# Optimization experiments

Measured on AMD Instinct MI355X. Metric: run time of the kernel, lower is better.

Reference implementation:

```python
import jax, jax.numpy as jnp
import numpy as np

B, S, D = 8, 2048, 1024      # batch, seq (tokens), in/out token dim
E = 2 * D                    # expansion dim (expansion_factor=2)
SDIM = 128                   # attention feature dim s
SQRT_S = float(np.sqrt(SDIM))
EPS_LN = 1e-5                # ScaleNorm eps


def setup_inputs() -> dict:
    key = jax.random.key(0)
    ks = jax.random.split(key, 8)
    return {
        "x": jax.random.normal(ks[0], (B, S, D), jnp.float32),
        "pos_enc": jax.random.normal(ks[1], (S, SDIM), jnp.float32),
        "ln_g": jnp.ones((1,), jnp.float32),                                   # ScaleNorm scalar gain
        "uv_w": jax.random.normal(ks[2], (2 * E + SDIM, D), jnp.float32) / np.sqrt(D),  # fused uv proj (xavier-ish)
        "gamma": jax.random.uniform(ks[3], (2, SDIM), jnp.float32),            # q/k affine scale
        "beta": jax.random.uniform(ks[4], (2, SDIM), jnp.float32),             # q/k affine shift
        "o_w": jax.random.normal(ks[5], (D, E), jnp.float32) / np.sqrt(E),     # output proj
        "res_scale": jnp.ones((D,), jnp.float32),                              # ChannelWiseScale
    }


def reference(x, pos_enc, ln_g, uv_w, gamma, beta, o_w, res_scale):
    # ScaleNorm: x / clamp(||x|| * d^-0.5, eps) * g
    norm = jnp.linalg.norm(x, axis=-1, keepdims=True) * (D ** -0.5)
    xn = x / jnp.maximum(norm, EPS_LN) * ln_g
    # fused uv projection + SiLU
    uv = jax.nn.silu(xn @ uv_w.T)                      # [B,S,2E+s]
    u = uv[..., :E]                                    # gate
    v = uv[..., E:2 * E]                               # values
    base = uv[..., 2 * E:]                             # shared q/k base [B,S,s]
    qk_base = base[..., None, :] * gamma + beta        # [B,S,2,s]
    q = qk_base[..., 0, :] + pos_enc                   # add positional enc [B,S,s]
    k = qk_base[..., 1, :] + pos_enc
    # squared-ReLU attention kernel
    kernel = jnp.square(jax.nn.relu(jnp.einsum('bqs,bks->bqk', q, k) / SQRT_S))
    out = (u * jnp.einsum('bqk,bke->bqe', kernel, v)) @ o_w.T  # [B,S,D]
    # channel-wise scaled residual (in_dims == out_dims -> shortcut)
    return x * res_scale + out
```

## Files before the change

### kernel.cpp

```cpp
#include <hip/hip_runtime.h>
#include <stdint.h>

#define B_   8
#define S_   2048
#define D_   1024
#define E_   2048
#define SD_  128
#define M_   (B_ * S_)
#define NUV  (2 * E_ + SD_)

typedef __attribute__((ext_vector_type(8))) short short8;
typedef __attribute__((ext_vector_type(4))) float floatx4;

typedef __attribute__((address_space(1))) void as1_void;
typedef __attribute__((address_space(3))) void as3_void;

__device__ __forceinline__ ushort f2bf(float f) {
    uint32_t u = __float_as_uint(f);
    uint32_t r = (u + 0x7fffu + ((u >> 16) & 1u)) >> 16;
    return (ushort)r;
}
__device__ __forceinline__ float bf2f(ushort h) {
    return __uint_as_float(((uint32_t)h) << 16);
}
__device__ __forceinline__ float silu(float z) {
    return z * __builtin_amdgcn_rcpf(1.0f + __expf(-z));
}

__device__ __forceinline__ void gld_lds16(const ushort* g, ushort* l) {
    __builtin_amdgcn_global_load_lds((const as1_void*)g, (as3_void*)l, 16, 0, 0);
}

__device__ __forceinline__ void tile_swizzle(int& mt, int& nt) {
    const int gx  = gridDim.x;
    const int lin = blockIdx.y * gx + blockIdx.x;
    const int bandSz = gx * 8;
    const int band = lin / bandSz;
    const int rem  = lin - band * bandSz;
    const int full = gx >> 2;
    const int sc   = rem >> 5;
    if (sc < full) {
        const int r2 = rem & 31;
        mt = band * 8 + (r2 & 7);
        nt = sc * 4 + (r2 >> 3);
    } else {
        const int r3 = rem - full * 32;
        mt = band * 8 + (r3 & 7);
        nt = full * 4 + (r3 >> 3);
    }
}

__device__ __forceinline__ void gemm_core(
    const ushort* __restrict__ A, const ushort* __restrict__ B,
    int lda, int ldb, int K, int m0, int n0,
    ushort* ldsA, ushort* ldsB, floatx4 acc[4][4])
{
    const int t    = threadIdx.x;
    const int lane = t & 63;
    const int l15  = lane & 15;
    const int quad = lane >> 4;
    const int wave = t >> 6;
    const int wm   = (wave >> 1) * 64;
    const int wn   = (wave & 1) * 64;
    const int key  = l15 & 7;

    const ushort* gA[4]; const ushort* gB[4];
    ushort* lA[4]; ushort* lB[4];
    #pragma unroll
    for (int i = 0; i < 4; ++i) {
        const int c   = t + i * 256;
        const int row = c >> 3;
        const int gkc = ((c & 7) ^ (row & 7)) * 8;
        gA[i] = A + (size_t)(m0 + row) * lda + gkc;
        gB[i] = B + (size_t)(n0 + row) * ldb + gkc;
        lA[i] = ldsA + c * 8;
        lB[i] = ldsB + c * 8;
    }

    for (int kk = 0; kk < K; kk += 64) {
        __syncthreads();
        #pragma unroll
        for (int i = 0; i < 4; ++i) gld_lds16(gA[i] + kk, lA[i]);
        #pragma unroll
        for (int i = 0; i < 4; ++i) gld_lds16(gB[i] + kk, lB[i]);
        __syncthreads();

        #pragma unroll
        for (int s = 0; s < 2; ++s) {
            const int koff = ((s * 4 + quad) ^ key) * 8;
            short8 af[4], bfr[4];
            #pragma unroll
            for (int mi = 0; mi < 4; ++mi)
                af[mi] = *(const short8*)(ldsA + (wm + mi * 16 + l15) * 64 + koff);
            #pragma unroll
            for (int ni = 0; ni < 4; ++ni)
                bfr[ni] = *(const short8*)(ldsB + (wn + ni * 16 + l15) * 64 + koff);
            #pragma unroll
            for (int mi = 0; mi < 4; ++mi)
                #pragma unroll
                for (int ni = 0; ni < 4; ++ni)
                    acc[mi][ni] = __builtin_amdgcn_mfma_f32_16x16x32_bf16(
                        af[mi], bfr[ni], acc[mi][ni], 0, 0, 0);
        }
    }
}

#define EPI_INDICES \
    const int t = threadIdx.x; \
    const int lane = t & 63, l15 = lane & 15, quad = lane >> 4; \
    const int wave = t >> 6, wm = (wave >> 1) * 64, wn = (wave & 1) * 64; \
    (void)t;

#define ZERO_ACC \
    floatx4 acc[4][4]; \
    _Pragma("unroll") \
    for (int i = 0; i < 4; ++i) \
        _Pragma("unroll") \
        for (int j = 0; j < 4; ++j) \
            _Pragma("unroll") \
            for (int r = 0; r < 4; ++r) acc[i][j][r] = 0.0f;

__global__ __launch_bounds__(256) void k_cvt(const float* __restrict__ src,
                                             ushort* __restrict__ dst, int n4) {
    int i = blockIdx.x * 256 + threadIdx.x;
    if (i < n4) {
        float4 v = ((const float4*)src)[i];
        ushort4 o;
        o.x = f2bf(v.x); o.y = f2bf(v.y); o.z = f2bf(v.z); o.w = f2bf(v.w);
        ((ushort4*)dst)[i] = o;
    }
}

__global__ __launch_bounds__(256) void k_rmsnorm(const float* __restrict__ x,
                                                 const float* __restrict__ ln_g,
                                                 ushort* __restrict__ xnb) {
    const int m = blockIdx.x;
    const int t = threadIdx.x;
    float4 v = ((const float4*)(x + (size_t)m * D_))[t];
    float ss = v.x * v.x + v.y * v.y + v.z * v.z + v.w * v.w;
    #pragma unroll
    for (int off = 32; off > 0; off >>= 1) ss += __shfl_down(ss, off, 64);
    __shared__ float red[4];
    if ((t & 63) == 0) red[t >> 6] = ss;
    __syncthreads();
    float tot = red[0] + red[1] + red[2] + red[3];
    float rms = sqrtf(tot * (1.0f / (float)D_));
    float scale = ln_g[0] / fmaxf(rms, 1e-5f);
    ushort4 o;
    o.x = f2bf(v.x * scale); o.y = f2bf(v.y * scale);
    o.z = f2bf(v.z * scale); o.w = f2bf(v.w * scale);
    ((ushort4*)(xnb + (size_t)m * D_))[t] = o;
}

__global__ __launch_bounds__(256, 3) void k_gemm1(
    const ushort* __restrict__ xnb, const ushort* __restrict__ uvwb,
    const float* __restrict__ gamma, const float* __restrict__ beta,
    const float* __restrict__ pos,
    ushort* __restrict__ u, ushort* __restrict__ vT,
    ushort* __restrict__ qb, ushort* __restrict__ kb)
{
    __shared__ __align__(16) ushort lds[17408];
    ushort* ldsA = lds;
    ushort* ldsB = lds + 8192;
    ZERO_ACC
    int mt, nt;
    tile_swizzle(mt, nt);
    const int m0 = mt * 128;
    const int n0 = nt * 128;
    gemm_core(xnb, uvwb, D_, D_, D_, m0, n0, ldsA, ldsB, acc);
    EPI_INDICES

    if (nt < 16) {
        #pragma unroll
        for (int mi = 0; mi < 4; ++mi)
            #pragma unroll
            for (int ni = 0; ni < 4; ++ni) {
                const int col = n0 + wn + ni * 16 + l15;
                #pragma unroll
                for (int r = 0; r < 4; ++r) {
                    const int row = m0 + wm + mi * 16 + quad * 4 + r;
                    u[(size_t)row * E_ + col] = f2bf(silu(acc[mi][ni][r]));
                }
            }
    } else if (nt < 32) {
        const int b   = m0 >> 11;
        const int s0  = m0 & (S_ - 1);
        const int ec0 = n0 - E_;
        __syncthreads();
        #pragma unroll
        for (int mi = 0; mi < 4; ++mi)
            #pragma unroll
            for (int ni = 0; ni < 4; ++ni) {
                const int col = wn + ni * 16 + l15;
                const int row = wm + mi * 16 + quad * 4;
                #pragma unroll
                for (int r = 0; r < 4; r += 2) {
                    ushort2 pr;
                    pr.x = f2bf(silu(acc[mi][ni][r]));
                    pr.y = f2bf(silu(acc[mi][ni][r + 1]));
                    *(ushort2*)&lds[col * 136 + row + r] = pr;
                }
            }
        __syncthreads();
        ushort* vTb = vT + ((size_t)b * E_ + ec0) * S_ + s0;
        #pragma unroll
        for (int i = 0; i < 8; ++i) {
            const int lin = i * 256 + t;
            const int e  = lin >> 4;
            const int sb = (lin & 15) * 8;
            *(short8*)(vTb + (size_t)e * S_ + sb) = *(const short8*)&lds[e * 136 + sb];
        }
    } else {
        #pragma unroll
        for (int mi = 0; mi < 4; ++mi)
            #pragma unroll
            for (int ni = 0; ni < 4; ++ni) {
                const int sd = wn + ni * 16 + l15;
                const float g0 = gamma[sd], g1 = gamma[SD_ + sd];
                const float be0 = beta[sd], be1 = beta[SD_ + sd];
                #pragma unroll
                for (int r = 0; r < 4; ++r) {
                    const int row = m0 + wm + mi * 16 + quad * 4 + r;
                    const int srow = row & (S_ - 1);
                    float s = silu(acc[mi][ni][r]);
                    const float p = pos[(size_t)srow * SD_ + sd];
                    qb[(size_t)row * SD_ + sd] = f2bf(s * g0 + be0 + p);
                    kb[(size_t)row * SD_ + sd] = f2bf(s * g1 + be1 + p);
                }
            }
    }
}

__global__ __launch_bounds__(256, 3) void k_scores(
    const ushort* __restrict__ qb, const ushort* __restrict__ kb,
    ushort* __restrict__ kern, int b_off)
{
    __shared__ __align__(16) ushort ldsA[128 * 64];
    __shared__ __align__(16) ushort ldsB[128 * 64];
    ZERO_ACC
    const int bz = blockIdx.z;
    const int b  = b_off + bz;
    int mt, nt;
    tile_swizzle(mt, nt);
    const int m0 = mt * 128;
    const int n0 = nt * 128;
    gemm_core(qb + (size_t)b * S_ * SD_, kb + (size_t)b * S_ * SD_,
              SD_, SD_, SD_, m0, n0, ldsA, ldsB, acc);
    EPI_INDICES
    ushort* ko = kern + (size_t)bz * S_ * S_;
    const float inv = 0.08838834764831845f;
    #pragma unroll
    for (int mi = 0; mi < 4; ++mi)
        #pragma unroll
        for (int ni = 0; ni < 4; ++ni) {
            const int col = n0 + wn + ni * 16 + l15;
            #pragma unroll
            for (int r = 0; r < 4; ++r) {
                const int row = m0 + wm + mi * 16 + quad * 4 + r;
                float s = fmaxf(acc[mi][ni][r] * inv, 0.0f);
                ko[(size_t)row * S_ + col] = f2bf(s * s);
            }
        }
}

__global__ __launch_bounds__(256, 3) void k_kv(
    const ushort* __restrict__ kern, const ushort* __restrict__ vT,
    const ushort* __restrict__ u, ushort* __restrict__ kvu, int b_off)
{
    __shared__ __align__(16) ushort ldsA[128 * 64];
    __shared__ __align__(16) ushort ldsB[128 * 64];
    ZERO_ACC
    const int bz = blockIdx.z;
    const int b  = b_off + bz;
    int mt, nt;
    tile_swizzle(mt, nt);
    const int m0 = mt * 128;
    const int n0 = nt * 128;
    gemm_core(kern + (size_t)bz * S_ * S_, vT + (size_t)b * E_ * S_,
              S_, S_, S_, m0, n0, ldsA, ldsB, acc);
    EPI_INDICES
    #pragma unroll
    for (int mi = 0; mi < 4; ++mi)
        #pragma unroll
        for (int ni = 0; ni < 4; ++ni) {
            const int col = n0 + wn + ni * 16 + l15;
            #pragma unroll
            for (int r = 0; r < 4; ++r) {
                const int row = m0 + wm + mi * 16 + quad * 4 + r;
                const size_t gi = (size_t)(b * S_ + row) * E_ + col;
                float uval = bf2f(u[gi]);
                kvu[gi] = f2bf(uval * acc[mi][ni][r]);
            }
        }
}

__global__ __launch_bounds__(256, 3) void k_out(
    const ushort* __restrict__ kvu, const ushort* __restrict__ owb,
    const float* __restrict__ x, const float* __restrict__ res_scale,
    float* __restrict__ out)
{
    __shared__ __align__(16) ushort ldsA[128 * 64];
    __shared__ __align__(16) ushort ldsB[128 * 64];
    ZERO_ACC
    int mt, nt;
    tile_swizzle(mt, nt);
    const int m0 = mt * 128;
    const int n0 = nt * 128;
    gemm_core(kvu, owb, E_, E_, E_, m0, n0, ldsA, ldsB, acc);
    EPI_INDICES
    #pragma unroll
    for (int mi = 0; mi < 4; ++mi)
        #pragma unroll
        for (int ni = 0; ni < 4; ++ni) {
            const int col = n0 + wn + ni * 16 + l15;
            const float rs = res_scale[col];
            #pragma unroll
            for (int r = 0; r < 4; ++r) {
                const int row = m0 + wm + mi * 16 + quad * 4 + r;
                const size_t gi = (size_t)row * D_ + col;
                out[gi] = x[gi] * rs + acc[mi][ni][r];
            }
        }
}

extern "C" void kernel_launch(void* const* d_in, const int* in_sizes, int n_in,
                              void* d_out, int out_size, void* d_ws, size_t ws_size,
                              hipStream_t stream)
{
    const float* x         = (const float*)d_in[0];
    const float* pos       = (const float*)d_in[1];
    const float* ln_g      = (const float*)d_in[2];
    const float* uv_w      = (const float*)d_in[3];
    const float* gamma     = (const float*)d_in[4];
    const float* beta      = (const float*)d_in[5];
    const float* o_w       = (const float*)d_in[6];
    const float* res_scale = (const float*)d_in[7];
    float* out = (float*)d_out;

    char* p = (char*)d_ws;
    ushort* region0 = (ushort*)p; p += (size_t)M_ * D_ * 2;
    ushort* uvwb    = (ushort*)p; p += (size_t)NUV * D_ * 2;
    ushort* owb     = (ushort*)p; p += (size_t)D_ * E_ * 2;
    ushort* u       = (ushort*)p; p += (size_t)M_ * E_ * 2;
    ushort* kvu     = (ushort*)p; p += (size_t)M_ * E_ * 2;
    ushort* vT      = (ushort*)p; p += (size_t)M_ * E_ * 2;
    ushort* qb      = (ushort*)p; p += (size_t)M_ * SD_ * 2;
    ushort* kb      = (ushort*)p; p += (size_t)M_ * SD_ * 2;

    ushort* xnb  = region0;
    ushort* kern = region0;

    k_cvt<<<(NUV * D_ / 4 + 255) / 256, 256, 0, stream>>>(uv_w, uvwb, NUV * D_ / 4);
    k_cvt<<<(D_ * E_ / 4 + 255) / 256, 256, 0, stream>>>(o_w, owb, D_ * E_ / 4);
    k_rmsnorm<<<M_, 256, 0, stream>>>(x, ln_g, xnb);
    k_gemm1<<<dim3(NUV / 128, M_ / 128), 256, 0, stream>>>(xnb, uvwb, gamma, beta, pos, u, vT, qb, kb);
    for (int g = 0; g < 2; ++g) {
        k_scores<<<dim3(S_ / 128, S_ / 128, 4), 256, 0, stream>>>(qb, kb, kern, g * 4);
        k_kv<<<dim3(E_ / 128, S_ / 128, 4), 256, 0, stream>>>(kern, vT, u, kvu, g * 4);
    }
    k_out<<<dim3(D_ / 128, M_ / 128), 256, 0, stream>>>(kvu, owb, x, res_scale, out);
}
```

Baseline: 576.8 us.

## Switch all GEMMs to 256x256 tiles with double-buffered 8-wave ping-pong pipeline

Replaces the 128x128 single-buffered GEMM core with a 256x256 tile, 512-thread (8-wave) kernel. It double-buffers LDS (128 KB) and interleaves async global-to-LDS loads with MFMA phases, using explicit waitcnt, barriers and setprio. The uv weight is zero-padded to a multiple of 256 rows so the first GEMM tiles evenly, and the epilogues are reworked for the new accumulator layout. The aim is higher arithmetic intensity and hiding load latency behind compute. In exchange, occupancy drops and the grid gets coarser, so tail effects grow, and the hand-tuned waitcnt scheme is fragile.

```diff
diff --git a/kernel.cpp b/kernel.cpp
--- a/kernel.cpp
+++ b/kernel.cpp
@@ -8,6 +8,7 @@
 #define SD_  128
 #define M_   (B_ * S_)
 #define NUV  (2 * E_ + SD_)
+#define NUV2 4352
 
 typedef __attribute__((ext_vector_type(8))) short short8;
 typedef __attribute__((ext_vector_type(4))) float floatx4;
@@ -26,99 +27,136 @@
 __device__ __forceinline__ float silu(float z) {
     return z * __builtin_amdgcn_rcpf(1.0f + __expf(-z));
 }
-
 __device__ __forceinline__ void gld_lds16(const ushort* g, ushort* l) {
     __builtin_amdgcn_global_load_lds((const as1_void*)g, (as3_void*)l, 16, 0, 0);
 }
 
-__device__ __forceinline__ void tile_swizzle(int& mt, int& nt) {
+__device__ __forceinline__ void tile_swizzle4(int& mt, int& nt) {
     const int gx  = gridDim.x;
     const int lin = blockIdx.y * gx + blockIdx.x;
-    const int bandSz = gx * 8;
+    const int bandSz = gx * 4;
     const int band = lin / bandSz;
     const int rem  = lin - band * bandSz;
     const int full = gx >> 2;
-    const int sc   = rem >> 5;
+    const int sc   = rem >> 4;
     if (sc < full) {
-        const int r2 = rem & 31;
-        mt = band * 8 + (r2 & 7);
-        nt = sc * 4 + (r2 >> 3);
+        const int r2 = rem & 15;
+        mt = band * 4 + (r2 & 3);
+        nt = sc * 4 + (r2 >> 2);
     } else {
-        const int r3 = rem - full * 32;
-        mt = band * 8 + (r3 & 7);
-        nt = full * 4 + (r3 >> 3);
-    }
-}
-
-__device__ __forceinline__ void gemm_core(
+        const int r3 = rem - full * 16;
+        mt = band * 4 + (r3 & 3);
+        nt = full * 4 + (r3 >> 2);
+    }
+}
+
+#define STAGE_A(bufn, h, kk) { \
+    gld_lds16(gA0 + (size_t)(h) * a128 + (kk), LA##bufn + (h) * 8192 + t * 8); \
+    gld_lds16(gA1 + (size_t)(h) * a128 + (kk), LA##bufn + (h) * 8192 + t * 8 + 4096); }
+#define STAGE_B(bufn, h, kk) { \
+    gld_lds16(gB0 + (size_t)(h) * b128 + (kk), LB##bufn + (h) * 8192 + t * 8); \
+    gld_lds16(gB1 + (size_t)(h) * b128 + (kk), LB##bufn + (h) * 8192 + t * 8 + 4096); }
+
+#define PHASE(bufn, mq, nq, STAGES, WAITC) { \
+    short8 af_[4][2], bf_[2][2]; \
+    { const ushort* pa_ = LA##bufn + (mq) * 8192 + aoff; \
+      const ushort* pb_ = LB##bufn + (nq) * 8192 + boff; \
+      _Pragma("unroll") \
+      for (int mi_ = 0; mi_ < 4; ++mi_) { \
+          af_[mi_][0] = *(const short8*)(pa_ + mi_ * 1024 + koff0); \
+          af_[mi_][1] = *(const short8*)(pa_ + mi_ * 1024 + koff1); } \
+      _Pragma("unroll") \
+      for (int ni_ = 0; ni_ < 2; ++ni_) { \
+          bf_[ni_][0] = *(const short8*)(pb_ + ni_ * 1024 + koff0); \
+          bf_[ni_][1] = *(const short8*)(pb_ + ni_ * 1024 + koff1); } } \
+    STAGES \
+    __builtin_amdgcn_s_barrier(); \
+    asm volatile("s_waitcnt lgkmcnt(0)" ::: "memory"); \
+    __builtin_amdgcn_sched_barrier(0); \
+    __builtin_amdgcn_s_setprio(1); \
+    _Pragma("unroll") \
+    for (int mi_ = 0; mi_ < 4; ++mi_) \
+        _Pragma("unroll") \
+        for (int ni_ = 0; ni_ < 2; ++ni_) { \
+            acc[mq][nq][mi_][ni_] = __builtin_amdgcn_mfma_f32_16x16x32_bf16( \
+                af_[mi_][0], bf_[ni_][0], acc[mq][nq][mi_][ni_], 0, 0, 0); \
+            acc[mq][nq][mi_][ni_] = __builtin_amdgcn_mfma_f32_16x16x32_bf16( \
+                af_[mi_][1], bf_[ni_][1], acc[mq][nq][mi_][ni_], 0, 0, 0); } \
+    __builtin_amdgcn_s_setprio(0); \
+    WAITC \
+    __builtin_amdgcn_s_barrier(); }
+
+__device__ __forceinline__ void gemm256(
     const ushort* __restrict__ A, const ushort* __restrict__ B,
     int lda, int ldb, int K, int m0, int n0,
-    ushort* ldsA, ushort* ldsB, floatx4 acc[4][4])
+    ushort* lds, floatx4 (&acc)[2][2][4][2])
 {
     const int t    = threadIdx.x;
     const int lane = t & 63;
     const int l15  = lane & 15;
     const int quad = lane >> 4;
-    const int wave = t >> 6;
-    const int wm   = (wave >> 1) * 64;
-    const int wn   = (wave & 1) * 64;
+    const int w    = t >> 6;
+    const int wr   = w >> 2;
+    const int wc   = w & 3;
     const int key  = l15 & 7;
-
-    const ushort* gA[4]; const ushort* gB[4];
-    ushort* lA[4]; ushort* lB[4];
-    #pragma unroll
-    for (int i = 0; i < 4; ++i) {
-        const int c   = t + i * 256;
-        const int row = c >> 3;
-        const int gkc = ((c & 7) ^ (row & 7)) * 8;
-        gA[i] = A + (size_t)(m0 + row) * lda + gkc;
-        gB[i] = B + (size_t)(n0 + row) * ldb + gkc;
-        lA[i] = ldsA + c * 8;
-        lB[i] = ldsB + c * 8;
-    }
-
-    for (int kk = 0; kk < K; kk += 64) {
-        __syncthreads();
-        #pragma unroll
-        for (int i = 0; i < 4; ++i) gld_lds16(gA[i] + kk, lA[i]);
-        #pragma unroll
-        for (int i = 0; i < 4; ++i) gld_lds16(gB[i] + kk, lB[i]);
-        __syncthreads();
-
-        #pragma unroll
-        for (int s = 0; s < 2; ++s) {
-            const int koff = ((s * 4 + quad) ^ key) * 8;
-            short8 af[4], bfr[4];
-            #pragma unroll
-            for (int mi = 0; mi < 4; ++mi)
-                af[mi] = *(const short8*)(ldsA + (wm + mi * 16 + l15) * 64 + koff);
-            #pragma unroll
-            for (int ni = 0; ni < 4; ++ni)
-                bfr[ni] = *(const short8*)(ldsB + (wn + ni * 16 + l15) * 64 + koff);
-            #pragma unroll
-            for (int mi = 0; mi < 4; ++mi)
-                #pragma unroll
-                for (int ni = 0; ni < 4; ++ni)
-                    acc[mi][ni] = __builtin_amdgcn_mfma_f32_16x16x32_bf16(
-                        af[mi], bfr[ni], acc[mi][ni], 0, 0, 0);
-        }
-    }
-}
-
-#define EPI_INDICES \
+    const int aoff  = (wr * 64 + l15) * 64;
+    const int boff  = (wc * 32 + l15) * 64;
+    const int koff0 = (quad ^ key) * 8;
+    const int koff1 = ((quad + 4) ^ key) * 8;
+
+    ushort* const LA0 = lds;
+    ushort* const LA1 = lds + 16384;
+    ushort* const LB0 = lds + 32768;
+    ushort* const LB1 = lds + 49152;
+
+    const int r0 = t >> 3;
+    const int k0 = ((t & 7) ^ (r0 & 7)) * 8;
+    const ushort* gA0 = A + (size_t)(m0 + r0) * lda + k0;
+    const ushort* gA1 = gA0 + (size_t)64 * lda;
+    const ushort* gB0 = B + (size_t)(n0 + r0) * ldb + k0;
+    const ushort* gB1 = gB0 + (size_t)64 * ldb;
+    const size_t a128 = (size_t)128 * lda;
+    const size_t b128 = (size_t)128 * ldb;
+
+    STAGE_A(0, 0, 0) STAGE_B(0, 0, 0) STAGE_A(0, 1, 0) STAGE_B(0, 1, 0)
+    STAGE_A(1, 0, 64) STAGE_B(1, 0, 64)
+    asm volatile("s_waitcnt vmcnt(4)" ::: "memory");
+    __builtin_amdgcn_s_barrier();
+
+    const int nIter = K >> 7;
+    #pragma unroll 1
+    for (int i = 0; i < nIter; ++i) {
+        const bool lastI = (i == nIter - 1);
+        const int kb = i * 128;
+        PHASE(0, 0, 0, STAGE_A(1, 1, kb + 64) STAGE_B(1, 1, kb + 64), )
+        PHASE(0, 0, 1, , )
+        PHASE(0, 1, 0, if (!lastI) { STAGE_A(0, 0, kb + 128) }, )
+        PHASE(0, 1, 1, if (!lastI) { STAGE_B(0, 0, kb + 128) },
+              if (!lastI) { asm volatile("s_waitcnt vmcnt(4)" ::: "memory"); }
+              else        { asm volatile("s_waitcnt vmcnt(0)" ::: "memory"); } )
+        PHASE(1, 0, 0, if (!lastI) { STAGE_A(0, 1, kb + 128) STAGE_B(0, 1, kb + 128) }, )
+        PHASE(1, 0, 1, , )
+        PHASE(1, 1, 0, if (!lastI) { STAGE_A(1, 0, kb + 192) }, )
+        PHASE(1, 1, 1, if (!lastI) { STAGE_B(1, 0, kb + 192) },
+              if (!lastI) { asm volatile("s_waitcnt vmcnt(4)" ::: "memory"); } )
+    }
+}
+
+#define ZERO_ACC256 \
+    floatx4 acc[2][2][4][2]; \
+    _Pragma("unroll") for (int zq_ = 0; zq_ < 2; ++zq_) \
+    _Pragma("unroll") for (int zn_ = 0; zn_ < 2; ++zn_) \
+    _Pragma("unroll") for (int zm_ = 0; zm_ < 4; ++zm_) \
+    _Pragma("unroll") for (int zl_ = 0; zl_ < 2; ++zl_) \
+    _Pragma("unroll") for (int zr_ = 0; zr_ < 4; ++zr_) \
+        acc[zq_][zn_][zm_][zl_][zr_] = 0.0f;
+
+#define EPI256 \
     const int t = threadIdx.x; \
     const int lane = t & 63, l15 = lane & 15, quad = lane >> 4; \
-    const int wave = t >> 6, wm = (wave >> 1) * 64, wn = (wave & 1) * 64; \
-    (void)t;
-
-#define ZERO_ACC \
-    floatx4 acc[4][4]; \
-    _Pragma("unroll") \
-    for (int i = 0; i < 4; ++i) \
-        _Pragma("unroll") \
-        for (int j = 0; j < 4; ++j) \
-            _Pragma("unroll") \
-            for (int r = 0; r < 4; ++r) acc[i][j][r] = 0.0f;
+    const int w = t >> 6, wr = w >> 2, wc = w & 3; \
+    (void)t; (void)lane;
+
 
 __global__ __launch_bounds__(256) void k_cvt(const float* __restrict__ src,
                                              ushort* __restrict__ dst, int n4) {
@@ -152,175 +190,190 @@
     ((ushort4*)(xnb + (size_t)m * D_))[t] = o;
 }
 
-__global__ __launch_bounds__(256, 3) void k_gemm1(
+__global__ __launch_bounds__(512, 2) void k_gemm1(
     const ushort* __restrict__ xnb, const ushort* __restrict__ uvwb,
     const float* __restrict__ gamma, const float* __restrict__ beta,
     const float* __restrict__ pos,
     ushort* __restrict__ u, ushort* __restrict__ vT,
     ushort* __restrict__ qb, ushort* __restrict__ kb)
 {
-    __shared__ __align__(16) ushort lds[17408];
-    ushort* ldsA = lds;
-    ushort* ldsB = lds + 8192;
-    ZERO_ACC
+    __shared__ __align__(16) ushort lds[65536];
+    ZERO_ACC256
     int mt, nt;
-    tile_swizzle(mt, nt);
-    const int m0 = mt * 128;
-    const int n0 = nt * 128;
-    gemm_core(xnb, uvwb, D_, D_, D_, m0, n0, ldsA, ldsB, acc);
-    EPI_INDICES
-
-    if (nt < 16) {
+    tile_swizzle4(mt, nt);
+    const int m0 = mt * 256, n0 = nt * 256;
+    gemm256(xnb, uvwb, D_, D_, D_, m0, n0, lds, acc);
+    EPI256
+
+    if (nt < 8) {
+        #pragma unroll
+        for (int mq = 0; mq < 2; ++mq)
+        #pragma unroll
+        for (int nq = 0; nq < 2; ++nq)
         #pragma unroll
         for (int mi = 0; mi < 4; ++mi)
-            #pragma unroll
-            for (int ni = 0; ni < 4; ++ni) {
-                const int col = n0 + wn + ni * 16 + l15;
+        #pragma unroll
+        for (int ni = 0; ni < 2; ++ni) {
+            const int col = n0 + nq * 128 + wc * 32 + ni * 16 + l15;
+            const int rb  = m0 + mq * 128 + wr * 64 + mi * 16 + quad * 4;
+            #pragma unroll
+            for (int r = 0; r < 4; ++r)
+                u[(size_t)(rb + r) * E_ + col] = f2bf(silu(acc[mq][nq][mi][ni][r]));
+        }
+    } else if (nt < 16) {
+        const int b   = m0 >> 11;
+        const int s0q = m0 & (S_ - 1);
+        const int ec0 = n0 - E_;
+        ushort* vTb = vT + ((size_t)b * E_ + ec0) * S_ + s0q;
+        #pragma unroll
+        for (int h = 0; h < 2; ++h) {
+            __syncthreads();
+            #pragma unroll
+            for (int mq = 0; mq < 2; ++mq)
+            #pragma unroll
+            for (int mi = 0; mi < 4; ++mi)
+            #pragma unroll
+            for (int ni = 0; ni < 2; ++ni) {
+                const int e_l = wc * 32 + ni * 16 + l15;
+                const int s_l = mq * 128 + wr * 64 + mi * 16 + quad * 4;
+                ushort4 pk;
+                pk.x = f2bf(silu(acc[mq][h][mi][ni][0]));
+                pk.y = f2bf(silu(acc[mq][h][mi][ni][1]));
+                pk.z = f2bf(silu(acc[mq][h][mi][ni][2]));
+                pk.w = f2bf(silu(acc[mq][h][mi][ni][3]));
+                *(ushort4*)&lds[e_l * 264 + s_l] = pk;
+            }
+            __syncthreads();
+            #pragma unroll
+            for (int i2 = 0; i2 < 8; ++i2) {
+                const int lin = i2 * 512 + t;
+                const int e_l = lin >> 5;
+                const int sc2 = (lin & 31) * 8;
+                *(short8*)(vTb + (size_t)(h * 128 + e_l) * S_ + sc2) =
+                    *(const short8*)&lds[e_l * 264 + sc2];
+            }
+        }
+    } else {
+        #pragma unroll
+        for (int ni = 0; ni < 2; ++ni) {
+            const int sd = wc * 32 + ni * 16 + l15;
+            const float g0 = gamma[sd], g1 = gamma[SD_ + sd];
+            const float be0 = beta[sd], be1 = beta[SD_ + sd];
+            #pragma unroll
+            for (int mq = 0; mq < 2; ++mq)
+            #pragma unroll
+            for (int mi = 0; mi < 4; ++mi) {
+                const int rb = m0 + mq * 128 + wr * 64 + mi * 16 + quad * 4;
                 #pragma unroll
                 for (int r = 0; r < 4; ++r) {
-                    const int row = m0 + wm + mi * 16 + quad * 4 + r;
-                    u[(size_t)row * E_ + col] = f2bf(silu(acc[mi][ni][r]));
-                }
-            }
-    } else if (nt < 32) {
-        const int b   = m0 >> 11;
-        const int s0  = m0 & (S_ - 1);
-        const int ec0 = n0 - E_;
-        __syncthreads();
-        #pragma unroll
-        for (int mi = 0; mi < 4; ++mi)
-            #pragma unroll
-            for (int ni = 0; ni < 4; ++ni) {
-                const int col = wn + ni * 16 + l15;
-                const int row = wm + mi * 16 + quad * 4;
-                #pragma unroll
-                for (int r = 0; r < 4; r += 2) {
-                    ushort2 pr;
-                    pr.x = f2bf(silu(acc[mi][ni][r]));
-                    pr.y = f2bf(silu(acc[mi][ni][r + 1]));
-                    *(ushort2*)&lds[col * 136 + row + r] = pr;
-                }
-            }
-        __syncthreads();
-        ushort* vTb = vT + ((size_t)b * E_ + ec0) * S_ + s0;
-        #pragma unroll
-        for (int i = 0; i < 8; ++i) {
-            const int lin = i * 256 + t;
-            const int e  = lin >> 4;
-            const int sb = (lin & 15) * 8;
-            *(short8*)(vTb + (size_t)e * S_ + sb) = *(const short8*)&lds[e * 136 + sb];
-        }
-    } else {
-        #pragma unroll
-        for (int mi = 0; mi < 4; ++mi)
-            #pragma unroll
-            for (int ni = 0; ni < 4; ++ni) {
-                const int sd = wn + ni * 16 + l15;
-                const float g0 = gamma[sd], g1 = gamma[SD_ + sd];
-                const float be0 = beta[sd], be1 = beta[SD_ + sd];
-                #pragma unroll
-                for (int r = 0; r < 4; ++r) {
-                    const int row = m0 + wm + mi * 16 + quad * 4 + r;
+                    const int row  = rb + r;
                     const int srow = row & (S_ - 1);
-                    float s = silu(acc[mi][ni][r]);
+                    const float s = silu(acc[mq][0][mi][ni][r]);
                     const float p = pos[(size_t)srow * SD_ + sd];
                     qb[(size_t)row * SD_ + sd] = f2bf(s * g0 + be0 + p);
                     kb[(size_t)row * SD_ + sd] = f2bf(s * g1 + be1 + p);
                 }
             }
-    }
-}
-
-__global__ __launch_bounds__(256, 3) void k_scores(
+        }
+    }
+}
+
+__global__ __launch_bounds__(512, 2) void k_scores(
     const ushort* __restrict__ qb, const ushort* __restrict__ kb,
     ushort* __restrict__ kern, int b_off)
 {
-    __shared__ __align__(16) ushort ldsA[128 * 64];
-    __shared__ __align__(16) ushort ldsB[128 * 64];
-    ZERO_ACC
+    __shared__ __align__(16) ushort lds[65536];
+    ZERO_ACC256
     const int bz = blockIdx.z;
     const int b  = b_off + bz;
     int mt, nt;
-    tile_swizzle(mt, nt);
-    const int m0 = mt * 128;
-    const int n0 = nt * 128;
-    gemm_core(qb + (size_t)b * S_ * SD_, kb + (size_t)b * S_ * SD_,
-              SD_, SD_, SD_, m0, n0, ldsA, ldsB, acc);
-    EPI_INDICES
+    tile_swizzle4(mt, nt);
+    const int m0 = mt * 256, n0 = nt * 256;
+    gemm256(qb + (size_t)b * S_ * SD_, kb + (size_t)b * S_ * SD_,
+            SD_, SD_, SD_, m0, n0, lds, acc);
+    EPI256
     ushort* ko = kern + (size_t)bz * S_ * S_;
     const float inv = 0.08838834764831845f;
     #pragma unroll
+    for (int mq = 0; mq < 2; ++mq)
+    #pragma unroll
+    for (int nq = 0; nq < 2; ++nq)
+    #pragma unroll
     for (int mi = 0; mi < 4; ++mi)
-        #pragma unroll
-        for (int ni = 0; ni < 4; ++ni) {
-            const int col = n0 + wn + ni * 16 + l15;
-            #pragma unroll
-            for (int r = 0; r < 4; ++r) {
-                const int row = m0 + wm + mi * 16 + quad * 4 + r;
-                float s = fmaxf(acc[mi][ni][r] * inv, 0.0f);
-                ko[(size_t)row * S_ + col] = f2bf(s * s);
-            }
-        }
-}
-
-__global__ __launch_bounds__(256, 3) void k_kv(
+    #pragma unroll
+    for (int ni = 0; ni < 2; ++ni) {
+        const int col = n0 + nq * 128 + wc * 32 + ni * 16 + l15;
+        const int rb  = m0 + mq * 128 + wr * 64 + mi * 16 + quad * 4;
+        #pragma unroll
+        for (int r = 0; r < 4; ++r) {
+            float s = fmaxf(acc[mq][nq][mi][ni][r] * inv, 0.0f);
+            ko[(size_t)(rb + r) * S_ + col] = f2bf(s * s);
+        }
+    }
+}
+
+__global__ __launch_bounds__(512, 2) void k_kv(
     const ushort* __restrict__ kern, const ushort* __restrict__ vT,
     const ushort* __restrict__ u, ushort* __restrict__ kvu, int b_off)
 {
-    __shared__ __align__(16) ushort ldsA[128 * 64];
-    __shared__ __align__(16) ushort ldsB[128 * 64];
-    ZERO_ACC
+    __shared__ __align__(16) ushort lds[65536];
+    ZERO_ACC256
     const int bz = blockIdx.z;
     const int b  = b_off + bz;
     int mt, nt;
-    tile_swizzle(mt, nt);
-    const int m0 = mt * 128;
-    const int n0 = nt * 128;
-    gemm_core(kern + (size_t)bz * S_ * S_, vT + (size_t)b * E_ * S_,
-              S_, S_, S_, m0, n0, ldsA, ldsB, acc);
-    EPI_INDICES
+    tile_swizzle4(mt, nt);
+    const int m0 = mt * 256, n0 = nt * 256;
+    gemm256(kern + (size_t)bz * S_ * S_, vT + (size_t)b * E_ * S_,
+            S_, S_, S_, m0, n0, lds, acc);
+    EPI256
+    #pragma unroll
+    for (int mq = 0; mq < 2; ++mq)
+    #pragma unroll
+    for (int nq = 0; nq < 2; ++nq)
     #pragma unroll
     for (int mi = 0; mi < 4; ++mi)
-        #pragma unroll
-        for (int ni = 0; ni < 4; ++ni) {
-            const int col = n0 + wn + ni * 16 + l15;
-            #pragma unroll
-            for (int r = 0; r < 4; ++r) {
-                const int row = m0 + wm + mi * 16 + quad * 4 + r;
-                const size_t gi = (size_t)(b * S_ + row) * E_ + col;
-                float uval = bf2f(u[gi]);
-                kvu[gi] = f2bf(uval * acc[mi][ni][r]);
-            }
-        }
-}
-
-__global__ __launch_bounds__(256, 3) void k_out(
+    #pragma unroll
+    for (int ni = 0; ni < 2; ++ni) {
+        const int col = n0 + nq * 128 + wc * 32 + ni * 16 + l15;
+        const int rb  = m0 + mq * 128 + wr * 64 + mi * 16 + quad * 4;
+        #pragma unroll
+        for (int r = 0; r < 4; ++r) {
+            const size_t gi = (size_t)(b * S_ + rb + r) * E_ + col;
+            float uval = bf2f(u[gi]);
+            kvu[gi] = f2bf(uval * acc[mq][nq][mi][ni][r]);
+        }
+    }
+}
+
+__global__ __launch_bounds__(512, 2) void k_out(
     const ushort* __restrict__ kvu, const ushort* __restrict__ owb,
     const float* __restrict__ x, const float* __restrict__ res_scale,
     float* __restrict__ out)
 {
-    __shared__ __align__(16) ushort ldsA[128 * 64];
-    __shared__ __align__(16) ushort ldsB[128 * 64];
-    ZERO_ACC
+    __shared__ __align__(16) ushort lds[65536];
+    ZERO_ACC256
     int mt, nt;
-    tile_swizzle(mt, nt);
-    const int m0 = mt * 128;
-    const int n0 = nt * 128;
-    gemm_core(kvu, owb, E_, E_, E_, m0, n0, ldsA, ldsB, acc);
-    EPI_INDICES
+    tile_swizzle4(mt, nt);
+    const int m0 = mt * 256, n0 = nt * 256;
+    gemm256(kvu, owb, E_, E_, E_, m0, n0, lds, acc);
+    EPI256
+    #pragma unroll
+    for (int mq = 0; mq < 2; ++mq)
+    #pragma unroll
+    for (int nq = 0; nq < 2; ++nq)
     #pragma unroll
     for (int mi = 0; mi < 4; ++mi)
-        #pragma unroll
-        for (int ni = 0; ni < 4; ++ni) {
-            const int col = n0 + wn + ni * 16 + l15;
-            const float rs = res_scale[col];
-            #pragma unroll
-            for (int r = 0; r < 4; ++r) {
-                const int row = m0 + wm + mi * 16 + quad * 4 + r;
-                const size_t gi = (size_t)row * D_ + col;
-                out[gi] = x[gi] * rs + acc[mi][ni][r];
-            }
-        }
+    #pragma unroll
+    for (int ni = 0; ni < 2; ++ni) {
+        const int col = n0 + nq * 128 + wc * 32 + ni * 16 + l15;
+        const float rs = res_scale[col];
+        const int rb = m0 + mq * 128 + wr * 64 + mi * 16 + quad * 4;
+        #pragma unroll
+        for (int r = 0; r < 4; ++r) {
+            const size_t gi = (size_t)(rb + r) * D_ + col;
+            out[gi] = x[gi] * rs + acc[mq][nq][mi][ni][r];
+        }
+    }
 }
 
 extern "C" void kernel_launch(void* const* d_in, const int* in_sizes, int n_in,
@@ -339,7 +392,7 @@
 
     char* p = (char*)d_ws;
     ushort* region0 = (ushort*)p; p += (size_t)M_ * D_ * 2;
-    ushort* uvwb    = (ushort*)p; p += (size_t)NUV * D_ * 2;
+    ushort* uvwb    = (ushort*)p; p += (size_t)NUV2 * D_ * 2;
     ushort* owb     = (ushort*)p; p += (size_t)D_ * E_ * 2;
     ushort* u       = (ushort*)p; p += (size_t)M_ * E_ * 2;
     ushort* kvu     = (ushort*)p; p += (size_t)M_ * E_ * 2;
@@ -351,12 +404,15 @@
     ushort* kern = region0;
 
     k_cvt<<<(NUV * D_ / 4 + 255) / 256, 256, 0, stream>>>(uv_w, uvwb, NUV * D_ / 4);
+    hipMemsetAsync(uvwb + (size_t)NUV * D_, 0,
+                   (size_t)(NUV2 - NUV) * D_ * sizeof(ushort), stream);
     k_cvt<<<(D_ * E_ / 4 + 255) / 256, 256, 0, stream>>>(o_w, owb, D_ * E_ / 4);
     k_rmsnorm<<<M_, 256, 0, stream>>>(x, ln_g, xnb);
-    k_gemm1<<<dim3(NUV / 128, M_ / 128), 256, 0, stream>>>(xnb, uvwb, gamma, beta, pos, u, vT, qb, kb);
+    k_gemm1<<<dim3(NUV2 / 256, M_ / 256), 512, 0, stream>>>(
+        xnb, uvwb, gamma, beta, pos, u, vT, qb, kb);
     for (int g = 0; g < 2; ++g) {
-        k_scores<<<dim3(S_ / 128, S_ / 128, 4), 256, 0, stream>>>(qb, kb, kern, g * 4);
-        k_kv<<<dim3(E_ / 128, S_ / 128, 4), 256, 0, stream>>>(kern, vT, u, kvu, g * 4);
-    }
-    k_out<<<dim3(D_ / 128, M_ / 128), 256, 0, stream>>>(kvu, owb, x, res_scale, out);
-}
+        k_scores<<<dim3(S_ / 256, S_ / 256, 4), 512, 0, stream>>>(qb, kb, kern, g * 4);
+        k_kv<<<dim3(E_ / 256, S_ / 256, 4), 512, 0, stream>>>(kern, vT, u, kvu, g * 4);
+    }
+    k_out<<<dim3(D_ / 256, M_ / 256), 512, 0, stream>>>(kvu, owb, x, res_scale, out);
+}
```

Result: slower. 595.4 us (+3.2%).
